# Kernel tuning notes

Hardware: AMD Instinct MI355X
Metric: run time of the kernel (lower is better)

Reference implementation:

```python
import jax, jax.numpy as jnp
import numpy as np

B = 8
M = 500_000
XSIZE = 128


def setup_inputs() -> dict:
    key = jax.random.key(0)
    k1, k2 = jax.random.split(key)
    indices = jax.random.randint(k1, (B, M, 3), 0, XSIZE, dtype=jnp.int32)
    values = jax.random.normal(k2, (B, M), dtype=jnp.float32)
    return {"indices": indices, "values": values, "xsize": XSIZE}


def reference(indices, values, xsize):
    # Batched scatter-add density accumulation (tensor_scatter_nd_add per sample)
    def scatter_one(idx, val):
        grid = jnp.zeros((xsize, xsize, xsize), dtype=val.dtype)
        return grid.at[idx[:, 0], idx[:, 1], idx[:, 2]].add(val)

    grid = jax.vmap(scatter_one)(indices, values)  # (B, X, X, X)

    # Adjacent voxel differences along each spatial axis
    d1 = grid[:, 1:, :, :] - grid[:, :-1, :, :]
    d2 = grid[:, :, 1:, :] - grid[:, :, :-1, :]
    d3 = grid[:, :, :, 1:] - grid[:, :, :, :-1]

    ax = (1, 2, 3)
    # Total variation loss: normalized by total voxel count xsize^3
    num_pixels = jnp.float32(xsize * xsize * xsize)
    tv = (jnp.sum(jnp.abs(d1), axis=ax)
          + jnp.sum(jnp.abs(d2), axis=ax)
          + jnp.sum(jnp.abs(d3), axis=ax)) / num_pixels

    # MSE smoothness loss: normalizer matches TF code (2*X*X - X - X)
    num_pairs = jnp.float32(2 * xsize * xsize - 2 * xsize)
    mse = (jnp.sum(jnp.square(d1), axis=ax)
           + jnp.sum(jnp.square(d2), axis=ax)
           + jnp.sum(jnp.square(d3), axis=ax)) / num_pairs

    return jnp.stack([tv, mse])  # (2, B)
```

## Files before the change

### kernel.cpp

```cpp
#include <hip/hip_runtime.h>
#include <stdint.h>

#define BATCH 8
#define MPTS 500000
#define NPTS (BATCH * MPTS)
#define NBQ 1024
#define TP 8192
#define NTILE ((NPTS + TP - 1) / TP)
#define HROW (NBQ + 1)
#define NIFACE 304
#define NBND (BATCH * NIFACE)

template <int NT>
__device__ __forceinline__ void block_reduce2(float& tv, float& mse) {
    for (int off = 32; off > 0; off >>= 1) {
        tv  += __shfl_down(tv, off, 64);
        mse += __shfl_down(mse, off, 64);
    }
    __shared__ float stv[NT / 64], sms[NT / 64];
    int w = threadIdx.x >> 6, lane = threadIdx.x & 63;
    if (lane == 0) { stv[w] = tv; sms[w] = mse; }
    __syncthreads();
    if (threadIdx.x == 0) {
        float a = 0.f, m = 0.f;
        #pragma unroll
        for (int e = 0; e < NT / 64; ++e) { a += stv[e]; m += sms[e]; }
        tv = a; mse = m;
    }
}

__device__ __forceinline__ uint32_t pack_aux(int b, int i, int j, int k) {
    uint32_t q = ((uint32_t)b << 7) | ((uint32_t)(i >> 5) << 5) |
                 ((uint32_t)(j >> 5) << 3) | (uint32_t)(k >> 4);
    uint32_t l = ((uint32_t)(i & 31) << 9) | ((uint32_t)(j & 31) << 4) | (uint32_t)(k & 15);
    return (q << 14) | l;
}

__device__ __forceinline__ int gaddr(int s, int kl) {
    return s * 16 + (kl & 3) + ((((kl >> 2) ^ (s >> 1)) & 3) << 2);
}
__device__ __forceinline__ int goff(int s, int c) {
    return ((c ^ (s >> 1)) & 3) << 2;
}

__device__ __forceinline__ uint32_t val16(float f) {
    return (__float_as_uint(f) + 0x8000u) >> 16;
}

__global__ void __launch_bounds__(1024, 8) sort_k(const int* __restrict__ idx,
                                                  const float* __restrict__ val,
                                                  uint16_t* __restrict__ hoff,
                                                  uint32_t* __restrict__ rec) {
    __shared__ uint32_t h[NBQ];
    __shared__ uint32_t wtot[16];
    __shared__ uint32_t srt[TP];
    int tile = blockIdx.x;
    int p0 = tile * TP;
    int cnt = min(TP, NPTS - p0);
    h[threadIdx.x] = 0;
    __syncthreads();
    uint32_t a[8]; uint32_t vpk[4];
    int ng = cnt >> 2;
    #pragma unroll
    for (int e = 0; e < 2; ++e) {
        int g = threadIdx.x + e * 1024;
        if (g < ng) {
            int p = p0 + g * 4;
            const int4* ip = (const int4*)(idx + (size_t)p * 3);
            int4 A = ip[0], B = ip[1], C = ip[2];
            float4 V = *(const float4*)(val + p);
            int b = p / MPTS;
            a[4*e+0] = pack_aux(b, A.x, A.y, A.z);
            a[4*e+1] = pack_aux(b, A.w, B.x, B.y);
            a[4*e+2] = pack_aux(b, B.z, B.w, C.x);
            a[4*e+3] = pack_aux(b, C.y, C.z, C.w);
            vpk[2*e]     = val16(V.x) | (val16(V.y) << 16);
            vpk[2*e + 1] = val16(V.z) | (val16(V.w) << 16);
            #pragma unroll
            for (int u = 0; u < 4; ++u) atomicAdd(&h[a[4*e+u] >> 14], 1u);
        } else {
            a[4*e+0] = a[4*e+1] = a[4*e+2] = a[4*e+3] = 0xFFFFFFFFu;
            vpk[2*e] = vpk[2*e + 1] = 0u;
        }
    }
    __syncthreads();
    int q = threadIdx.x, lane = q & 63, wave = q >> 6;
    uint32_t cq = h[q];
    uint32_t inc = cq;
    #pragma unroll
    for (int off = 1; off < 64; off <<= 1) {
        uint32_t n = __shfl_up(inc, off, 64);
        if (lane >= off) inc += n;
    }
    if (lane == 63) wtot[wave] = inc;
    __syncthreads();
    if (q < 16) {
        uint32_t w = wtot[q];
        #pragma unroll
        for (int off = 1; off < 16; off <<= 1) {
            uint32_t n = __shfl_up(w, off, 16);
            if (q >= off) w += n;
        }
        wtot[q] = w;
    }
    __syncthreads();
    uint32_t lstart = (wave ? wtot[wave - 1] : 0u) + inc - cq;
    hoff[(size_t)tile * HROW + q] = (uint16_t)lstart;
    if (q == 0) hoff[(size_t)tile * HROW + NBQ] = (uint16_t)cnt;
    h[q] = lstart;
    __syncthreads();
    #pragma unroll
    for (int e = 0; e < 8; ++e) {
        if (a[e] != 0xFFFFFFFFu) {
            uint32_t qq = a[e] >> 14;
            uint32_t u = (vpk[e >> 1] >> ((e & 1) * 16)) & 0xFFFFu;
            srt[atomicAdd(&h[qq], 1u)] = (u << 16) | (a[e] & 16383u);
        }
    }
    __syncthreads();
    uint4* recq = (uint4*)(rec + (size_t)tile * TP);
    const uint4* sr4 = (const uint4*)srt;
    for (int s = threadIdx.x; s < (cnt >> 2); s += 1024) recq[s] = sr4[s];
}

__global__ void __launch_bounds__(1024, 8) accum_k(const uint32_t* __restrict__ rec,
                                                   const uint16_t* __restrict__ hoff,
                                                   uint16_t* __restrict__ faces,
                                                   float2* __restrict__ pa) {
    __shared__ float g[16384];
    int qb = blockIdx.x;
    {
        float4 z = make_float4(0.f, 0.f, 0.f, 0.f);
        #pragma unroll
        for (int c = 0; c < 4; ++c)
            *(float4*)&g[(threadIdx.x + c * 1024) * 4] = z;
    }
    __syncthreads();
    {
        int grp = threadIdx.x >> 3;
        int r8  = threadIdx.x & 7;
        for (int t = grp; t < NTILE; t += 128) {
            const uint16_t* row = hoff + (size_t)t * HROW;
            uint32_t a0 = row[qb], a1 = row[qb + 1];
            const uint32_t* rp = rec + (size_t)t * TP;
            for (uint32_t r = a0 + r8; r < a1; r += 8) {
                uint32_t e = rp[r];
                int l = e & 16383;
                atomicAdd(&g[gaddr(l >> 4, l & 15)], __uint_as_float(e & 0xFFFF0000u));
            }
        }
    }
    __syncthreads();
    float tv = 0.f, mse = 0.f;
    {
        int s = threadIdx.x;
        int jl = s & 31, il = s >> 5;
        bool jin = jl < 31, iin = il < 31;
        float own[16];
        #pragma unroll
        for (int c = 0; c < 4; ++c)
            *(float4*)&own[c * 4] = *(const float4*)&g[s * 16 + goff(s, c)];
        #pragma unroll
        for (int k = 0; k < 15; ++k) {
            float d = own[k + 1] - own[k]; tv += fabsf(d); mse += d * d;
        }
        #pragma unroll
        for (int hh = 0; hh < 2; ++hh) {
            if (jin) {
                float jn[8];
                *(float4*)&jn[0] = *(const float4*)&g[(s + 1) * 16 + goff(s + 1, 2 * hh)];
                *(float4*)&jn[4] = *(const float4*)&g[(s + 1) * 16 + goff(s + 1, 2 * hh + 1)];
                #pragma unroll
                for (int k = 0; k < 8; ++k) {
                    float d = jn[k] - own[8 * hh + k]; tv += fabsf(d); mse += d * d;
                }
            }
            if (iin) {
                float inb[8];
                *(float4*)&inb[0] = *(const float4*)&g[(s + 32) * 16 + goff(s + 32, 2 * hh)];
                *(float4*)&inb[4] = *(const float4*)&g[(s + 32) * 16 + goff(s + 32, 2 * hh + 1)];
                #pragma unroll
                for (int k = 0; k < 8; ++k) {
                    float d = inb[k] - own[8 * hh + k]; tv += fabsf(d); mse += d * d;
                }
            }
        }
    }
    {
        uint16_t* f = faces + (size_t)qb * 4096;
        int t = threadIdx.x;
        if (t < 512) {
            int hi = t >> 4, lo = t & 15;
            f[t]        = (uint16_t)(__float_as_uint(g[gaddr(hi, lo)]) >> 16);
            f[512 + t]  = (uint16_t)(__float_as_uint(g[gaddr(992 + hi, lo)]) >> 16);
            f[1024 + t] = (uint16_t)(__float_as_uint(g[gaddr(hi * 32, lo)]) >> 16);
            f[1536 + t] = (uint16_t)(__float_as_uint(g[gaddr(hi * 32 + 31, lo)]) >> 16);
        }
        f[2048 + t] = (uint16_t)(__float_as_uint(g[gaddr(t, 0)]) >> 16);
        f[3072 + t] = (uint16_t)(__float_as_uint(g[gaddr(t, 15)]) >> 16);
    }
    block_reduce2<1024>(tv, mse);
    if (threadIdx.x == 0) pa[qb] = make_float2(tv, mse);
}

__device__ __forceinline__ float f16up(uint16_t u) {
    return __uint_as_float(((uint32_t)u) << 16);
}

__global__ void __launch_bounds__(256) boundary_k(const uint16_t* __restrict__ faces,
                                                  float2* __restrict__ pb) {
    int x = blockIdx.x;
    int b = x / NIFACE;
    int r = x - b * NIFACE;
    int qA, qB, fA, fB, elems;
    if (r < 96) {
        int s = r >> 5, u = (r >> 3) & 3, w = r & 7;
        qA = (b << 7) | (s << 5) | (u << 3) | w; qB = qA + 32;
        fA = 512; fB = 0; elems = 512;
    } else if (r < 192) {
        int r2 = r - 96;
        int s = r2 >> 5, u = (r2 >> 3) & 3, w = r2 & 7;
        qA = (b << 7) | (u << 5) | (s << 3) | w; qB = qA + 8;
        fA = 1536; fB = 1024; elems = 512;
    } else {
        int r2 = r - 192;
        int s = r2 >> 4, u = (r2 >> 2) & 3, v = r2 & 3;
        qA = (b << 7) | (u << 5) | (v << 3) | s; qB = qA + 1;
        fA = 3072; fB = 2048; elems = 1024;
    }
    const uint16_t* pA = faces + (size_t)qA * 4096 + fA;
    const uint16_t* pB = faces + (size_t)qB * 4096 + fB;
    float tv = 0.f, mse = 0.f;
    for (int e = threadIdx.x; e < elems; e += 256) {
        float d = f16up(pB[e]) - f16up(pA[e]);
        tv += fabsf(d); mse += d * d;
    }
    block_reduce2<256>(tv, mse);
    if (threadIdx.x == 0) pb[x] = make_float2(tv, mse);
}

__global__ void __launch_bounds__(256) final_k(const float2* __restrict__ pa,
                                               const float2* __restrict__ pb,
                                               float* __restrict__ out) {
    int b = blockIdx.x;
    float tv = 0.f, mse = 0.f;
    const float2* a = pa + (size_t)b * (NBQ / BATCH);
    for (int i = threadIdx.x; i < NBQ / BATCH; i += 256) { float2 v = a[i]; tv += v.x; mse += v.y; }
    const float2* p = pb + (size_t)b * NIFACE;
    for (int i = threadIdx.x; i < NIFACE; i += 256) { float2 v = p[i]; tv += v.x; mse += v.y; }
    block_reduce2<256>(tv, mse);
    if (threadIdx.x == 0) {
        out[b]     = tv  * (1.f / 2097152.f);
        out[8 + b] = mse * (1.f / 32512.f);
    }
}

extern "C" void kernel_launch(void* const* d_in, const int* in_sizes, int n_in,
                              void* d_out, int out_size, void* d_ws, size_t ws_size,
                              hipStream_t stream) {
    const int*   indices = (const int*)d_in[0];
    const float* values  = (const float*)d_in[1];
    float*       out     = (float*)d_out;

    char* wp = (char*)d_ws;
    uint16_t* hoff  = (uint16_t*)wp;
    wp += (((size_t)NTILE * HROW * 2) + 255) & ~(size_t)255;
    float2*   pa    = (float2*)wp;
    wp += (NBQ * 8 + 255) & ~(size_t)255;
    float2*   pb    = (float2*)wp;
    wp += ((size_t)NBND * 8 + 255) & ~(size_t)255;
    uint32_t* rec   = (uint32_t*)wp;
    wp += (((size_t)NTILE * TP * 4) + 255) & ~(size_t)255;
    uint16_t* faces = (uint16_t*)wp;

    sort_k    <<<NTILE, 1024, 0, stream>>>(indices, values, hoff, rec);
    accum_k   <<<NBQ,   1024, 0, stream>>>(rec, hoff, faces, pa);
    boundary_k<<<NBND,  256,  0, stream>>>(faces, pb);
    final_k   <<<BATCH, 256,  0, stream>>>(pa, pb, out);
}
```

Measured before the change: 137.3 us.

## Bucket records into global per-bucket slots via atomic cursors

The sort kernel no longer writes per-tile histogram offsets and tile-ordered records. Each tile now reserves space in a fixed-capacity per-bucket slot in global memory with an atomicAdd on a bucket cursor, and writes its zero-padded, 4-aligned segment there with uint4 stores. Accum blocks then read one contiguous region with vectorized loads instead of walking every tile's offset row. A block index swizzle is also added to accum. The cost is scattered small writes in the sort kernel, an extra memset, and a fixed slot capacity that assumes roughly uniform bucket occupancy and would overflow on skewed inputs.

```diff
diff --git a/kernel.cpp b/kernel.cpp
--- a/kernel.cpp
+++ b/kernel.cpp
@@ -7,7 +7,8 @@
 #define NBQ 1024
 #define TP 8192
 #define NTILE ((NPTS + TP - 1) / TP)
-#define HROW (NBQ + 1)
+#define RSLOT 5376
+#define CSTR 16
 #define NIFACE 304
 #define NBND (BATCH * NIFACE)
 
@@ -46,10 +47,13 @@
 __device__ __forceinline__ uint32_t val16(float f) {
     return (__float_as_uint(f) + 0x8000u) >> 16;
 }
+__device__ __forceinline__ float f16up(uint16_t u) {
+    return __uint_as_float(((uint32_t)u) << 16);
+}
 
 __global__ void __launch_bounds__(1024, 8) sort_k(const int* __restrict__ idx,
                                                   const float* __restrict__ val,
-                                                  uint16_t* __restrict__ hoff,
+                                                  uint32_t* __restrict__ gcur,
                                                   uint32_t* __restrict__ rec) {
     __shared__ uint32_t h[NBQ];
     __shared__ uint32_t wtot[16];
@@ -86,6 +90,8 @@
     __syncthreads();
     int q = threadIdx.x, lane = q & 63, wave = q >> 6;
     uint32_t cq = h[q];
+    uint32_t cq4 = (cq + 3u) & ~3u;
+    uint32_t gpos = atomicAdd(&gcur[q * CSTR], cq4);
     uint32_t inc = cq;
     #pragma unroll
     for (int off = 1; off < 64; off <<= 1) {
@@ -105,8 +111,6 @@
     }
     __syncthreads();
     uint32_t lstart = (wave ? wtot[wave - 1] : 0u) + inc - cq;
-    hoff[(size_t)tile * HROW + q] = (uint16_t)lstart;
-    if (q == 0) hoff[(size_t)tile * HROW + NBQ] = (uint16_t)cnt;
     h[q] = lstart;
     __syncthreads();
     #pragma unroll
@@ -118,17 +122,25 @@
         }
     }
     __syncthreads();
-    uint4* recq = (uint4*)(rec + (size_t)tile * TP);
-    const uint4* sr4 = (const uint4*)srt;
-    for (int s = threadIdx.x; s < (cnt >> 2); s += 1024) recq[s] = sr4[s];
+    {
+        uint32_t wbase = (uint32_t)q * RSLOT + gpos;
+        for (uint32_t n = 0; n < cq4; n += 4) {
+            uint4 w;
+            w.x = (n + 0 < cq) ? srt[lstart + n + 0] : 0u;
+            w.y = (n + 1 < cq) ? srt[lstart + n + 1] : 0u;
+            w.z = (n + 2 < cq) ? srt[lstart + n + 2] : 0u;
+            w.w = (n + 3 < cq) ? srt[lstart + n + 3] : 0u;
+            *(uint4*)(rec + wbase + n) = w;
+        }
+    }
 }
 
 __global__ void __launch_bounds__(1024, 8) accum_k(const uint32_t* __restrict__ rec,
-                                                   const uint16_t* __restrict__ hoff,
+                                                   const uint32_t* __restrict__ gcur,
                                                    uint16_t* __restrict__ faces,
                                                    float2* __restrict__ pa) {
     __shared__ float g[16384];
-    int qb = blockIdx.x;
+    int qb = ((blockIdx.x & 7) << 7) | (blockIdx.x >> 3);
     {
         float4 z = make_float4(0.f, 0.f, 0.f, 0.f);
         #pragma unroll
@@ -137,14 +149,14 @@
     }
     __syncthreads();
     {
-        int grp = threadIdx.x >> 3;
-        int r8  = threadIdx.x & 7;
-        for (int t = grp; t < NTILE; t += 128) {
-            const uint16_t* row = hoff + (size_t)t * HROW;
-            uint32_t a0 = row[qb], a1 = row[qb + 1];
-            const uint32_t* rp = rec + (size_t)t * TP;
-            for (uint32_t r = a0 + r8; r < a1; r += 8) {
-                uint32_t e = rp[r];
+        uint32_t count4 = gcur[qb * CSTR];
+        const uint32_t* rp = rec + (size_t)qb * RSLOT;
+        for (uint32_t r = threadIdx.x * 4; r < count4; r += 4096) {
+            uint4 e4 = *(const uint4*)(rp + r);
+            uint32_t es[4] = {e4.x, e4.y, e4.z, e4.w};
+            #pragma unroll
+            for (int u = 0; u < 4; ++u) {
+                uint32_t e = es[u];
                 int l = e & 16383;
                 atomicAdd(&g[gaddr(l >> 4, l & 15)], __uint_as_float(e & 0xFFFF0000u));
             }
@@ -201,10 +213,6 @@
     }
     block_reduce2<1024>(tv, mse);
     if (threadIdx.x == 0) pa[qb] = make_float2(tv, mse);
-}
-
-__device__ __forceinline__ float f16up(uint16_t u) {
-    return __uint_as_float(((uint32_t)u) << 16);
 }
 
 __global__ void __launch_bounds__(256) boundary_k(const uint16_t* __restrict__ faces,
@@ -263,18 +271,19 @@
     float*       out     = (float*)d_out;
 
     char* wp = (char*)d_ws;
-    uint16_t* hoff  = (uint16_t*)wp;
-    wp += (((size_t)NTILE * HROW * 2) + 255) & ~(size_t)255;
+    uint32_t* gcur  = (uint32_t*)wp;
+    wp += ((size_t)NBQ * CSTR * 4 + 255) & ~(size_t)255;
     float2*   pa    = (float2*)wp;
     wp += (NBQ * 8 + 255) & ~(size_t)255;
     float2*   pb    = (float2*)wp;
     wp += ((size_t)NBND * 8 + 255) & ~(size_t)255;
     uint32_t* rec   = (uint32_t*)wp;
-    wp += (((size_t)NTILE * TP * 4) + 255) & ~(size_t)255;
+    wp += (((size_t)NBQ * RSLOT * 4) + 255) & ~(size_t)255;
     uint16_t* faces = (uint16_t*)wp;
 
-    sort_k    <<<NTILE, 1024, 0, stream>>>(indices, values, hoff, rec);
-    accum_k   <<<NBQ,   1024, 0, stream>>>(rec, hoff, faces, pa);
+    hipMemsetAsync(gcur, 0, (size_t)NBQ * CSTR * 4, stream);
+    sort_k    <<<NTILE, 1024, 0, stream>>>(indices, values, gcur, rec);
+    accum_k   <<<NBQ,   1024, 0, stream>>>(rec, gcur, faces, pa);
     boundary_k<<<NBND,  256,  0, stream>>>(faces, pb);
     final_k   <<<BATCH, 256,  0, stream>>>(pa, pb, out);
 }
```

Result: slower. 154.1 us (+12.2%).
